# Optimization experiments

Hardware: AMD Instinct MI355X
Metric: run time of the kernel (lower is better)

The kernel has to match this reference:

```python
import jax, jax.numpy as jnp
import numpy as np

BS, M, CLIP_DIM = 64, 1000, 512
D = 512
N_WAYS = 20
N_Z = 8


def setup_inputs() -> dict:
    key = jax.random.key(0)
    ks = jax.random.split(key, 16)
    s = 0.02
    inp = {
        "x_context": jax.random.normal(ks[0], (BS, M, CLIP_DIM), jnp.float32),
        "y_context": jax.random.randint(ks[1], (BS, M), 0, N_WAYS),
        "x_query": jax.random.normal(ks[2], (BS, M, CLIP_DIM), jnp.float32),
        # image_proj
        "Wp": jax.random.normal(ks[3], (CLIP_DIM, D), jnp.float32) * s,
        "bp": jnp.zeros((D,), jnp.float32),
        # aggregator: Linear(d,d) -> GELU -> Linear(d,2d)
        "Wa1": jax.random.normal(ks[4], (D, D), jnp.float32) * s,
        "ba1": jnp.zeros((D,), jnp.float32),
        "Wa2": jax.random.normal(ks[5], (D, 2 * D), jnp.float32) * s,
        "ba2": jnp.zeros((2 * D,), jnp.float32),
        # decoder: Linear(d,d) -> GELU -> Linear(d,d)
        "Wd1": jax.random.normal(ks[6], (D, D), jnp.float32) * s,
        "bd1": jnp.zeros((D,), jnp.float32),
        "Wd2": jax.random.normal(ks[7], (D, D), jnp.float32) * s,
        "bd2": jnp.zeros((D,), jnp.float32),
    }
    return inp


def reference(x_context, y_context, x_query, Wp, bp, Wa1, ba1, Wa2, ba2, Wd1, bd1, Wd2, bd2):
    # project image embeddings: [bs, M, clip_dim] -> [bs, M, d]
    xc = x_context @ Wp + bp
    xq = x_query @ Wp + bp

    # encode_context_per_class: per-class masked sum == one-hot segment-sum
    # (original loops over classes doing (x*mask).sum(dim=1))
    oh = jax.nn.one_hot(y_context, N_WAYS, dtype=xc.dtype)  # [bs, M, N]
    r_C = jnp.einsum('bmn,bmd->bnd', oh, xc)  # [bs, N, d]

    # knowledge is None -> k = zeros; combined = relu(r + 0)
    combined = jax.nn.relu(r_C)
    h = jax.nn.gelu(combined @ Wa1 + ba1, approximate=False)
    stats = h @ Wa2 + ba2  # [bs, N, 2d]
    mu, scale_raw = stats[..., :D], stats[..., D:]
    scale = 0.01 + 0.99 * jax.nn.softplus(scale_raw)

    # eval path: sample n_z from q(z|C) via reparameterization
    eps = jax.random.normal(jax.random.key(42), (N_Z,) + mu.shape, mu.dtype)
    z_samples = mu[None] + scale[None] * eps  # [n_z, bs, N, d]

    # decode: class weight vectors then inner product with queries
    W = jax.nn.gelu(z_samples @ Wd1 + bd1, approximate=False) @ Wd2 + bd2
    logits = jnp.einsum('bqd,sbnd->sbqn', xq, W)  # [n_z, bs, Q*N, N]
    return logits, z_samples, mu, scale
```

## Files before the change

kernel.cpp:

```cpp
#include <hip/hip_runtime.h>
#include <hip/hip_bf16.h>
#include <stdint.h>


typedef __attribute__((ext_vector_type(8))) short short8;
typedef __attribute__((ext_vector_type(4))) float f32x4;

__device__ __forceinline__ float gelu_f(float x) {
    return 0.5f * x * (1.0f + erff(x * 0.70710678118654752440f));
}
__device__ __forceinline__ float softplus_f(float x) {
    return fmaxf(x, 0.0f) + log1pf(expf(-fabsf(x)));
}
__device__ __forceinline__ uint32_t cvt2(float a, float b) {
    __hip_bfloat162 h;
    h.x = __float2bfloat16(a);
    h.y = __float2bfloat16(b);
    uint32_t u; __builtin_memcpy(&u, &h, 4); return u;
}
__device__ __forceinline__ unsigned short f2bfu(float f) {
    __hip_bfloat16 h = __float2bfloat16(f);
    unsigned short u; __builtin_memcpy(&u, &h, 2); return u;
}
__device__ __forceinline__ float bfu2f(unsigned short u) {
    uint32_t v = (uint32_t)u << 16; float f; __builtin_memcpy(&f, &v, 4); return f;
}

__device__ __forceinline__ void threefry2x32(uint32_t k0, uint32_t k1,
                                             uint32_t x0, uint32_t x1,
                                             uint32_t& o0, uint32_t& o1) {
    uint32_t ks[3] = {k0, k1, k0 ^ k1 ^ 0x1BD11BDAu};
    x0 += ks[0]; x1 += ks[1];
    const uint32_t rot[8] = {13,15,26,6,17,29,16,24};
#pragma unroll
    for (int i = 0; i < 5; i++) {
#pragma unroll
        for (int j = 0; j < 4; j++) {
            uint32_t r = rot[(i & 1) * 4 + j];
            x0 += x1;
            x1 = (x1 << r) | (x1 >> (32 - r));
            x1 ^= x0;
        }
        x0 += ks[(i + 1) % 3];
        x1 += ks[(i + 2) % 3] + (uint32_t)(i + 1);
    }
    o0 = x0; o1 = x1;
}

__device__ __forceinline__ float bits_to_normal(uint32_t b) {
    float f = __uint_as_float((b >> 9) | 0x3F800000u) - 1.0f;
    const float lo = __uint_as_float(0xBF7FFFFFu);
    float u = fmaxf(lo, f * 2.0f + lo);
    return 1.41421356237309504880f * erfinvf(u);
}

__global__ __launch_bounds__(256) void prep_k(
    const float* __restrict__ Wp, const float* __restrict__ Wa1,
    const float* __restrict__ Wa2, const float* __restrict__ Wd1,
    const float* __restrict__ Wd2, const float* __restrict__ bp,
    const float* __restrict__ bd2, const int* __restrict__ y,
    unsigned short* __restrict__ WpTb, unsigned short* __restrict__ Wa1Tb,
    unsigned short* __restrict__ Wa2Tb, unsigned short* __restrict__ WdT1b,
    unsigned short* __restrict__ Wpb, unsigned short* __restrict__ Wd2b,
    float* __restrict__ bv, float* __restrict__ w2bp,
    float* __restrict__ c0, float* __restrict__ cnt)
{
    __shared__ float T[64][65];
    __shared__ int lc[32];
    __shared__ float ws4[4];
    const int f = blockIdx.x;
    const int tid = threadIdx.x;

    if (f < 320) {
        const float* src; unsigned short* dst; int C, t, xb, yb;
        if (f < 64)       { src = Wp;  dst = WpTb;  C = 512;  t = f;       xb = t & 7;  yb = t >> 3; }
        else if (f < 128) { src = Wa1; dst = Wa1Tb; C = 512;  t = f - 64;  xb = t & 7;  yb = t >> 3; }
        else if (f < 256) { src = Wa2; dst = Wa2Tb; C = 1024; t = f - 128; xb = t & 15; yb = t >> 4; }
        else              { src = Wd1; dst = WdT1b; C = 512;  t = f - 256; xb = t & 7;  yb = t >> 3; }
        const int r0 = yb * 64, cc0 = xb * 64;
        const int rr = tid >> 4, cc = (tid & 15) * 4;
#pragma unroll
        for (int l = 0; l < 4; l++) {
            int row = rr + l * 16;
            float4 v = *(const float4*)&src[(size_t)(r0 + row) * C + cc0 + cc];
            T[row][cc] = v.x; T[row][cc+1] = v.y; T[row][cc+2] = v.z; T[row][cc+3] = v.w;
        }
        __syncthreads();
#pragma unroll
        for (int l = 0; l < 4; l++) {
            int n = rr + l * 16;
            uint2 u;
            u.x = cvt2(T[cc][n], T[cc+1][n]);
            u.y = cvt2(T[cc+2][n], T[cc+3][n]);
            *(uint2*)&dst[(size_t)(cc0 + n) * 512 + r0 + cc] = u;
        }
    } else if (f < 576) {
        const float* src = (f < 448) ? Wp : Wd2;
        unsigned short* dst = (f < 448) ? Wpb : Wd2b;
        int t = (f < 448) ? f - 320 : f - 448;
        size_t i = ((size_t)t * 256 + tid) * 8;
        float4 a = *(const float4*)&src[i];
        float4 b4 = *(const float4*)&src[i + 4];
        uint4 u;
        u.x = cvt2(a.x, a.y);  u.y = cvt2(a.z, a.w);
        u.z = cvt2(b4.x, b4.y); u.w = cvt2(b4.z, b4.w);
        *(uint4*)&dst[i] = u;
    } else if (f < 832) {
        const float* W = (f < 704) ? Wp : Wd2;
        const float* v = (f < 704) ? bd2 : bp;
        float* o = (f < 704) ? bv : w2bp;
        int t = (f < 704) ? f - 576 : f - 704;
        int wave = tid >> 6, lane = tid & 63;
        int r = t * 4 + wave;
        const float* row = W + (size_t)r * 512 + lane * 8;
        float4 x0 = *(const float4*)row;
        float4 x1 = *(const float4*)(row + 4);
        float4 v0 = *(const float4*)&v[lane * 8];
        float4 v1 = *(const float4*)&v[lane * 8 + 4];
        float s = x0.x*v0.x + x0.y*v0.y + x0.z*v0.z + x0.w*v0.w
                + x1.x*v1.x + x1.y*v1.y + x1.z*v1.z + x1.w*v1.w;
#pragma unroll
        for (int off = 32; off > 0; off >>= 1) s += __shfl_down(s, off, 64);
        if (lane == 0) o[r] = s;
    } else if (f == 832) {
        float s = bp[tid] * bd2[tid] + bp[tid + 256] * bd2[tid + 256];
#pragma unroll
        for (int off = 32; off > 0; off >>= 1) s += __shfl_down(s, off, 64);
        int wave = tid >> 6, lane = tid & 63;
        if (lane == 0) ws4[wave] = s;
        __syncthreads();
        if (tid == 0) c0[0] = ws4[0] + ws4[1] + ws4[2] + ws4[3];
    } else {
        int b = f - 833;
        if (tid < 32) lc[tid] = 0;
        __syncthreads();
        for (int m = tid; m < 1000; m += 256)
            atomicAdd(&lc[y[b * 1000 + m]], 1);
        __syncthreads();
        if (tid < 20) cnt[b * 20 + tid] = (float)lc[tid];
    }
}

__global__ __launch_bounds__(256) void onehot_k(const float* __restrict__ xc,
                                                const int* __restrict__ y,
                                                unsigned short* __restrict__ Abf) {
    __shared__ unsigned short Xs[128 * 64];
    __shared__ int ys[1024];
    const int chb = blockIdx.x * 128;
    const int b = blockIdx.y;
    const int tid = threadIdx.x, lane = tid & 63, w = tid >> 6;
    const int chs = w * 32;

    for (int i = tid; i < 1024; i += 256)
        ys[i] = (i < 1000) ? y[b * 1000 + i] : -1;

    f32x4 acc[2][2] = {};
    for (int step = 0; step < 16; step++) {
        const int k0 = step * 64;
        int m = k0 + lane; if (m > 999) m = 999;
        const float* src = xc + ((size_t)b * 1000 + m) * 512 + chb + chs;
        float x[32];
#pragma unroll
        for (int j8 = 0; j8 < 8; j8++) {
            float4 v = *(const float4*)(src + j8 * 4);
            x[j8*4+0]=v.x; x[j8*4+1]=v.y; x[j8*4+2]=v.z; x[j8*4+3]=v.w;
        }
        __syncthreads();
#pragma unroll
        for (int j = 0; j < 32; j++) {
            int ch = chs + j;
            *(unsigned short*)((char*)Xs + ch * 128 + ((lane * 2) ^ ((ch & 7) << 4)))
                = f2bfu(x[j]);
        }
        __syncthreads();
#pragma unroll
        for (int ks = 0; ks < 2; ks++) {
            int kb = ks * 32 + (lane >> 4) * 8;
            int4 yv0 = *(const int4*)&ys[k0 + kb];
            int4 yv1 = *(const int4*)&ys[k0 + kb + 4];
            int ya[8] = {yv0.x, yv0.y, yv0.z, yv0.w, yv1.x, yv1.y, yv1.z, yv1.w};
            short8 a[2];
#pragma unroll
            for (int mi = 0; mi < 2; mi++) {
                int cls = mi * 16 + (lane & 15);
#pragma unroll
                for (int e = 0; e < 8; e++)
                    a[mi][e] = (short)((ya[e] == cls) ? 0x3F80 : 0);
            }
            short8 bb[2];
#pragma unroll
            for (int ni = 0; ni < 2; ni++) {
                int ch = chs + ni * 16 + (lane & 15);
                bb[ni] = *(const short8*)((const char*)Xs + ch * 128 +
                           ((kb * 2) ^ ((ch & 7) << 4)));
            }
#pragma unroll
            for (int mi = 0; mi < 2; mi++)
#pragma unroll
                for (int ni = 0; ni < 2; ni++)
                    acc[mi][ni] = __builtin_amdgcn_mfma_f32_16x16x32_bf16(a[mi], bb[ni], acc[mi][ni], 0, 0, 0);
        }
    }
#pragma unroll
    for (int mi = 0; mi < 2; mi++) {
#pragma unroll
        for (int ni = 0; ni < 2; ni++) {
            int ch = chb + chs + ni * 16 + (lane & 15);
#pragma unroll
            for (int j = 0; j < 4; j++) {
                int cls = mi * 16 + (lane >> 4) * 4 + j;
                if (cls < 20)
                    Abf[((size_t)b * 20 + cls) * 512 + ch] = f2bfu(acc[mi][ni][j]);
            }
        }
    }
}

template <int EPI>
__global__ __launch_bounds__(256) void gm2_k(const unsigned short* __restrict__ Abf,
                                             const unsigned short* __restrict__ Bbf,
                                             const float* __restrict__ bias,
                                             const float* __restrict__ extra,
                                             unsigned short* __restrict__ C0,
                                             float* __restrict__ F0,
                                             float* __restrict__ F1,
                                             int Nn) {
    __shared__ unsigned short As[64 * 64];
    __shared__ unsigned short Bs[128 * 64];
    const int tid = threadIdx.x;
    const int lane = tid & 63, w = tid >> 6;
    const int row0 = blockIdx.y * 64, col0 = blockIdx.x * 128;
    f32x4 acc[4][2] = {};
    for (int k0 = 0; k0 < 512; k0 += 64) {
        {
            int row = tid >> 2, cs = (tid & 3) * 16;
            int swz = (row & 7) << 4;
            const unsigned short* src = Abf + (size_t)(row0 + row) * 512 + k0 + cs;
#pragma unroll
            for (int j = 0; j < 2; j++) {
                uint4 u = *(const uint4*)(src + j * 8);
                *(uint4*)((char*)As + row * 128 + (((cs + j * 8) * 2) ^ swz)) = u;
            }
        }
        {
            int row = tid >> 1, cs = (tid & 1) * 32;
            int swz = (row & 7) << 4;
            const unsigned short* src = Bbf + (size_t)(col0 + row) * 512 + k0 + cs;
#pragma unroll
            for (int j = 0; j < 4; j++) {
                uint4 u = *(const uint4*)(src + j * 8);
                *(uint4*)((char*)Bs + row * 128 + (((cs + j * 8) * 2) ^ swz)) = u;
            }
        }
        __syncthreads();
#pragma unroll
        for (int ks = 0; ks < 2; ks++) {
            short8 a[4], bb[2];
#pragma unroll
            for (int mi = 0; mi < 4; mi++) {
                int r = mi * 16 + (lane & 15);
                a[mi] = *(const short8*)((const char*)As + r * 128 +
                          (((ks * 32 + (lane >> 4) * 8) * 2) ^ ((r & 7) << 4)));
            }
#pragma unroll
            for (int ni = 0; ni < 2; ni++) {
                int n = w * 32 + ni * 16 + (lane & 15);
                bb[ni] = *(const short8*)((const char*)Bs + n * 128 +
                          (((ks * 32 + (lane >> 4) * 8) * 2) ^ ((n & 7) << 4)));
            }
#pragma unroll
            for (int mi = 0; mi < 4; mi++)
#pragma unroll
                for (int ni = 0; ni < 2; ni++)
                    acc[mi][ni] = __builtin_amdgcn_mfma_f32_16x16x32_bf16(a[mi], bb[ni], acc[mi][ni], 0, 0, 0);
        }
        __syncthreads();
    }
#pragma unroll
    for (int mi = 0; mi < 4; mi++) {
#pragma unroll
        for (int ni = 0; ni < 2; ni++) {
            int c = col0 + w * 32 + ni * 16 + (lane & 15);
            float bvv = bias ? bias[c] : 0.f;
#pragma unroll
            for (int j = 0; j < 4; j++) {
                int r = row0 + mi * 16 + (lane >> 4) * 4 + j;
                float v = acc[mi][ni][j];
                if (EPI == 0) {
                    v += bvv;
                    C0[(size_t)r * Nn + c] = f2bfu(v);
                } else if (EPI == 1) {
                    v += extra[r] * bvv;
                    C0[(size_t)r * Nn + c] = f2bfu(fmaxf(v, 0.f));
                } else if (EPI == 2) {
                    C0[(size_t)r * Nn + c] = f2bfu(gelu_f(v + bvv));
                } else {
                    v += bvv;
                    if (c < 512) F0[(size_t)r * 512 + c] = v;
                    else F1[(size_t)r * 512 + (c - 512)] = 0.01f + 0.99f * softplus_f(v);
                }
            }
        }
    }
}

__global__ __launch_bounds__(256) void z2_k(const float* __restrict__ mu,
                                            const float* __restrict__ sc,
                                            float* __restrict__ z,
                                            unsigned short* __restrict__ zb) {
    const uint32_t NH = 2621440u;
    uint32_t i = blockIdx.x * 256u + threadIdx.x;
    if (i >= NH) return;
    uint32_t t0 = 2u * i;
    uint32_t o0, o1, p0, p1;
    threefry2x32(0u, 42u, 0u, t0, o0, o1);
    threefry2x32(0u, 42u, 0u, t0 + 1u, p0, p1);
    uint32_t r0 = t0 % 655360u;
    float2 mv = *(const float2*)&mu[r0];
    float2 sv = *(const float2*)&sc[r0];
    float z0 = mv.x + sv.x * bits_to_normal(o0 ^ o1);
    float z1 = mv.y + sv.y * bits_to_normal(p0 ^ p1);
    float2 zo; zo.x = z0; zo.y = z1;
    *(float2*)&z[t0] = zo;
    *(uint32_t*)&zb[t0] = cvt2(z0, z1);
}

__global__ __launch_bounds__(256) void beta2_k(const unsigned short* __restrict__ Wgb,
                                               const float* __restrict__ vec,
                                               const float* __restrict__ c0,
                                               float* __restrict__ beta) {
    int wave = threadIdx.x >> 6, lane = threadIdx.x & 63;
    int r = blockIdx.x * 4 + wave;
    short8 wv = *(const short8*)(Wgb + (size_t)r * 512 + lane * 8);
    float s = 0.f;
#pragma unroll
    for (int e = 0; e < 8; e++) s += vec[lane * 8 + e] * bfu2f((unsigned short)wv[e]);
#pragma unroll
    for (int o = 32; o > 0; o >>= 1) s += __shfl_down(s, o, 64);
    if (lane == 0) beta[r] = s + c0[0];
}

__global__ __launch_bounds__(512) void logits_mfma3_k(const float* __restrict__ Xq,
                                                      const unsigned short* __restrict__ Vb,
                                                      const float* __restrict__ beta,
                                                      float* __restrict__ out) {
    __shared__ unsigned short Vs[160 * 64];
    __shared__ float bs[160];
    const int u = blockIdx.x + 8 * blockIdx.y;
    const int xcd = u & 7, idx = u >> 3;
    const int b = (idx & 7) * 8 + xcd;
    const int qh = idx >> 3;
    const int tid = threadIdx.x, lane = tid & 63, w = tid >> 6;
    const int wq = w >> 1, wn = w & 1;

    if (tid < 160) {
        int s = tid / 20, n = tid - s * 20;
        bs[tid] = beta[(size_t)(s * 64 + b) * 20 + n];
    }

    const int klane = (lane >> 4) * 8;
    const float* xp[2];
    int qb[2];
#pragma unroll
    for (int qs = 0; qs < 2; qs++) {
        qb[qs] = qh * 128 + wq * 32 + qs * 16;
        int qr = qb[qs] + (lane & 15);
        if (qr > 999) qr = 999;
        xp[qs] = Xq + ((size_t)b * 1000 + qr) * 512 + klane;
    }
    int vrow[5], vswz[5];
#pragma unroll
    for (int nf = 0; nf < 5; nf++) {
        int rr = wn * 80 + nf * 16 + (lane & 15);
        vrow[nf] = rr * 128;
        vswz[nf] = (rr & 7) << 4;
    }

    f32x4 acc[2][5] = {};
    for (int k0 = 0; k0 < 512; k0 += 64) {
        __syncthreads();
        for (int c = tid; c < 640; c += 512) {
            int row = c >> 2, off = (c & 3) * 32;
            int sdiv = row / 20;
            int row_g = row + sdiv * 1260 + b * 20;
            const unsigned short* src = Vb + (size_t)row_g * 512 + k0 + (c & 3) * 16;
            uint4 u0 = *(const uint4*)src;
            uint4 u1 = *(const uint4*)(src + 8);
            int swz = (row & 7) << 4;
            char* base = (char*)Vs + row * 128;
            *(uint4*)(base + (off ^ swz)) = u0;
            *(uint4*)(base + ((off + 16) ^ swz)) = u1;
        }
        __syncthreads();
#pragma unroll
        for (int ks = 0; ks < 2; ks++) {
            int kb = (ks * 32 + klane) * 2;
            short8 bf[5];
#pragma unroll
            for (int nf = 0; nf < 5; nf++)
                bf[nf] = *(const short8*)((const char*)Vs + vrow[nf] + (kb ^ vswz[nf]));
            short8 af[2];
#pragma unroll
            for (int qs = 0; qs < 2; qs++) {
                const float* p = xp[qs] + k0 + ks * 32;
                float4 v0 = *(const float4*)p;
                float4 v1 = *(const float4*)(p + 4);
                uint4 uu;
                uu.x = cvt2(v0.x, v0.y); uu.y = cvt2(v0.z, v0.w);
                uu.z = cvt2(v1.x, v1.y); uu.w = cvt2(v1.z, v1.w);
                __builtin_memcpy(&af[qs], &uu, 16);
            }
#pragma unroll
            for (int qs = 0; qs < 2; qs++)
#pragma unroll
                for (int nf = 0; nf < 5; nf++)
                    acc[qs][nf] = __builtin_amdgcn_mfma_f32_16x16x32_bf16(af[qs], bf[nf], acc[qs][nf], 0, 0, 0);
        }
    }

#pragma unroll
    for (int nf = 0; nf < 5; nf++) {
        int rl = wn * 80 + nf * 16 + (lane & 15);
        int s = rl / 20, n = rl - s * 20;
        float bb = bs[rl];
        size_t ob = (size_t)(s * 64 + b) * 20000;
#pragma unroll
        for (int qs = 0; qs < 2; qs++) {
#pragma unroll
            for (int j = 0; j < 4; j++) {
                int q = qb[qs] + (lane >> 4) * 4 + j;
                if (q < 1000)
                    out[ob + (size_t)q * 20 + n] = acc[qs][nf][j] + bb;
            }
        }
    }
}

extern "C" void kernel_launch(void* const* d_in, const int* in_sizes, int n_in,
                              void* d_out, int out_size, void* d_ws, size_t ws_size,
                              hipStream_t stream) {
    const float* x_context = (const float*)d_in[0];
    const int*   y_context = (const int*)d_in[1];
    const float* x_query   = (const float*)d_in[2];
    const float* Wp  = (const float*)d_in[3];
    const float* bp  = (const float*)d_in[4];
    const float* Wa1 = (const float*)d_in[5];
    const float* ba1 = (const float*)d_in[6];
    const float* Wa2 = (const float*)d_in[7];
    const float* ba2 = (const float*)d_in[8];
    const float* Wd1 = (const float*)d_in[9];
    const float* bd1 = (const float*)d_in[10];
    const float* Wd2 = (const float*)d_in[11];
    const float* bd2 = (const float*)d_in[12];

    float* out    = (float*)d_out;
    float* logits = out;
    float* z      = out + 10240000;
    float* mu     = out + 15482880;
    float* sc     = out + 16138240;

    float* ws   = (float*)d_ws;
    float* cnt  = ws;
    float* beta = cnt + 1280;
    float* bv   = beta + 10240;
    float* w2bp = bv + 512;
    float* c0   = w2bp + 512;
    unsigned short* WpTb  = (unsigned short*)(c0 + 63);
    unsigned short* Wa1Tb = WpTb + 262144;
    unsigned short* Wa2Tb = Wa1Tb + 262144;
    unsigned short* WdT1b = Wa2Tb + 524288;
    unsigned short* Wpb   = WdT1b + 262144;
    unsigned short* Wd2b  = Wpb + 262144;
    unsigned short* Gtb   = Wd2b + 262144;
    unsigned short* Abf   = Gtb + 262144;
    unsigned short* combb = Abf + 655360;
    unsigned short* hb    = combb + 655360;
    unsigned short* zb    = hb + 655360;
    unsigned short* Vbf   = zb + 5242880;
    float* big = (float*)(Vbf + 5242880);
    unsigned short* Wgb = (unsigned short*)big;

    prep_k<<<dim3(897), 256, 0, stream>>>(Wp, Wa1, Wa2, Wd1, Wd2, bp, bd2, y_context,
                                          WpTb, Wa1Tb, Wa2Tb, WdT1b, Wpb, Wd2b,
                                          bv, w2bp, c0, cnt);
    gm2_k<0><<<dim3(4, 8), 256, 0, stream>>>(Wpb, Wd2b, nullptr, nullptr, Gtb, nullptr, nullptr, 512);
    onehot_k<<<dim3(4, 64), 256, 0, stream>>>(x_context, y_context, Abf);
    gm2_k<1><<<dim3(4, 20), 256, 0, stream>>>(Abf, WpTb, bp, cnt, combb, nullptr, nullptr, 512);
    gm2_k<2><<<dim3(4, 20), 256, 0, stream>>>(combb, Wa1Tb, ba1, nullptr, hb, nullptr, nullptr, 512);
    gm2_k<3><<<dim3(8, 20), 256, 0, stream>>>(hb, Wa2Tb, ba2, nullptr, nullptr, mu, sc, 1024);
    z2_k<<<dim3(10240), 256, 0, stream>>>(mu, sc, z, zb);
    gm2_k<2><<<dim3(4, 160), 256, 0, stream>>>(zb, WdT1b, bd1, nullptr, Wgb, nullptr, nullptr, 512);
    gm2_k<0><<<dim3(4, 160), 256, 0, stream>>>(Wgb, Gtb, bv, nullptr, Vbf, nullptr, nullptr, 512);
    beta2_k<<<dim3(2560), 256, 0, stream>>>(Wgb, w2bp, c0, beta);
    logits_mfma3_k<<<dim3(8, 64), 512, 0, stream>>>(x_query, Vbf, beta, logits);
}
```

Before: 232.0 us.

## Split one-hot segment-sum over M chunks and fuse weight conversion into Gt GEMM

The one-hot class-sum kernel now splits the 1000 context rows into four chunks, launching 1024 blocks instead of 256 to raise occupancy. Each chunk writes fp32 partials, and a new reduction kernel sums them and converts to bf16. Separately, the Wp·Wd2 product GEMM now reads fp32 weights directly and converts them to bf16 while loading tiles, removing the separate conversion pass in prep_k. The cost is an extra kernel launch and a partial-sum buffer round-trip through global memory.

```diff
diff --git a/kernel.cpp b/kernel.cpp
--- a/kernel.cpp
+++ b/kernel.cpp
@@ -61,7 +61,6 @@
     const float* __restrict__ bd2, const int* __restrict__ y,
     unsigned short* __restrict__ WpTb, unsigned short* __restrict__ Wa1Tb,
     unsigned short* __restrict__ Wa2Tb, unsigned short* __restrict__ WdT1b,
-    unsigned short* __restrict__ Wpb, unsigned short* __restrict__ Wd2b,
     float* __restrict__ bv, float* __restrict__ w2bp,
     float* __restrict__ c0, float* __restrict__ cnt)
 {
@@ -95,21 +94,10 @@
             *(uint2*)&dst[(size_t)(cc0 + n) * 512 + r0 + cc] = u;
         }
     } else if (f < 576) {
-        const float* src = (f < 448) ? Wp : Wd2;
-        unsigned short* dst = (f < 448) ? Wpb : Wd2b;
+        const float* W = (f < 448) ? Wp : Wd2;
+        const float* v = (f < 448) ? bd2 : bp;
+        float* o = (f < 448) ? bv : w2bp;
         int t = (f < 448) ? f - 320 : f - 448;
-        size_t i = ((size_t)t * 256 + tid) * 8;
-        float4 a = *(const float4*)&src[i];
-        float4 b4 = *(const float4*)&src[i + 4];
-        uint4 u;
-        u.x = cvt2(a.x, a.y);  u.y = cvt2(a.z, a.w);
-        u.z = cvt2(b4.x, b4.y); u.w = cvt2(b4.z, b4.w);
-        *(uint4*)&dst[i] = u;
-    } else if (f < 832) {
-        const float* W = (f < 704) ? Wp : Wd2;
-        const float* v = (f < 704) ? bd2 : bp;
-        float* o = (f < 704) ? bv : w2bp;
-        int t = (f < 704) ? f - 576 : f - 704;
         int wave = tid >> 6, lane = tid & 63;
         int r = t * 4 + wave;
         const float* row = W + (size_t)r * 512 + lane * 8;
@@ -122,7 +110,7 @@
 #pragma unroll
         for (int off = 32; off > 0; off >>= 1) s += __shfl_down(s, off, 64);
         if (lane == 0) o[r] = s;
-    } else if (f == 832) {
+    } else if (f == 576) {
         float s = bp[tid] * bd2[tid] + bp[tid + 256] * bd2[tid + 256];
 #pragma unroll
         for (int off = 32; off > 0; off >>= 1) s += __shfl_down(s, off, 64);
@@ -131,7 +119,7 @@
         __syncthreads();
         if (tid == 0) c0[0] = ws4[0] + ws4[1] + ws4[2] + ws4[3];
     } else {
-        int b = f - 833;
+        int b = f - 577;
         if (tid < 32) lc[tid] = 0;
         __syncthreads();
         for (int m = tid; m < 1000; m += 256)
@@ -141,23 +129,102 @@
     }
 }
 
-__global__ __launch_bounds__(256) void onehot_k(const float* __restrict__ xc,
-                                                const int* __restrict__ y,
-                                                unsigned short* __restrict__ Abf) {
+__global__ __launch_bounds__(256) void gmG_k(const float* __restrict__ Ap,
+                                             const float* __restrict__ Bp,
+                                             unsigned short* __restrict__ C) {
+    __shared__ unsigned short As[64 * 64];
+    __shared__ unsigned short Bs[128 * 64];
+    const int tid = threadIdx.x;
+    const int lane = tid & 63, w = tid >> 6;
+    const int row0 = blockIdx.y * 64, col0 = blockIdx.x * 128;
+    f32x4 acc[4][2] = {};
+    for (int k0 = 0; k0 < 512; k0 += 64) {
+        {
+            int row = tid >> 2, cs = (tid & 3) * 16;
+            int swz = (row & 7) << 4;
+            const float* src = Ap + (size_t)(row0 + row) * 512 + k0 + cs;
+#pragma unroll
+            for (int j = 0; j < 2; j++) {
+                float4 v0 = *(const float4*)(src + j * 8);
+                float4 v1 = *(const float4*)(src + j * 8 + 4);
+                uint4 u;
+                u.x = cvt2(v0.x, v0.y); u.y = cvt2(v0.z, v0.w);
+                u.z = cvt2(v1.x, v1.y); u.w = cvt2(v1.z, v1.w);
+                *(uint4*)((char*)As + row * 128 + (((cs + j * 8) * 2) ^ swz)) = u;
+            }
+        }
+        {
+            int row = tid >> 1, cs = (tid & 1) * 32;
+            int swz = (row & 7) << 4;
+            const float* src = Bp + (size_t)(col0 + row) * 512 + k0 + cs;
+#pragma unroll
+            for (int j = 0; j < 4; j++) {
+                float4 v0 = *(const float4*)(src + j * 8);
+                float4 v1 = *(const float4*)(src + j * 8 + 4);
+                uint4 u;
+                u.x = cvt2(v0.x, v0.y); u.y = cvt2(v0.z, v0.w);
+                u.z = cvt2(v1.x, v1.y); u.w = cvt2(v1.z, v1.w);
+                *(uint4*)((char*)Bs + row * 128 + (((cs + j * 8) * 2) ^ swz)) = u;
+            }
+        }
+        __syncthreads();
+#pragma unroll
+        for (int ks = 0; ks < 2; ks++) {
+            short8 a[4], bb[2];
+#pragma unroll
+            for (int mi = 0; mi < 4; mi++) {
+                int r = mi * 16 + (lane & 15);
+                a[mi] = *(const short8*)((const char*)As + r * 128 +
+                          (((ks * 32 + (lane >> 4) * 8) * 2) ^ ((r & 7) << 4)));
+            }
+#pragma unroll
+            for (int ni = 0; ni < 2; ni++) {
+                int n = w * 32 + ni * 16 + (lane & 15);
+                bb[ni] = *(const short8*)((const char*)Bs + n * 128 +
+                          (((ks * 32 + (lane >> 4) * 8) * 2) ^ ((n & 7) << 4)));
+            }
+#pragma unroll
+            for (int mi = 0; mi < 4; mi++)
+#pragma unroll
+                for (int ni = 0; ni < 2; ni++)
+                    acc[mi][ni] = __builtin_amdgcn_mfma_f32_16x16x32_bf16(a[mi], bb[ni], acc[mi][ni], 0, 0, 0);
+        }
+        __syncthreads();
+    }
+#pragma unroll
+    for (int mi = 0; mi < 4; mi++)
+#pragma unroll
+        for (int ni = 0; ni < 2; ni++) {
+            int c = col0 + w * 32 + ni * 16 + (lane & 15);
+#pragma unroll
+            for (int j = 0; j < 4; j++) {
+                int r = row0 + mi * 16 + (lane >> 4) * 4 + j;
+                C[(size_t)r * 512 + c] = f2bfu(acc[mi][ni][j]);
+            }
+        }
+}
+
+__global__ __launch_bounds__(256) void onehot4_k(const float* __restrict__ xc,
+                                                 const int* __restrict__ y,
+                                                 float* __restrict__ Apart) {
     __shared__ unsigned short Xs[128 * 64];
-    __shared__ int ys[1024];
+    __shared__ int ys[256];
     const int chb = blockIdx.x * 128;
-    const int b = blockIdx.y;
+    const int mc = blockIdx.y;
+    const int b = blockIdx.z;
+    const int m00 = mc * 256;
     const int tid = threadIdx.x, lane = tid & 63, w = tid >> 6;
     const int chs = w * 32;
 
-    for (int i = tid; i < 1024; i += 256)
-        ys[i] = (i < 1000) ? y[b * 1000 + i] : -1;
+    {
+        int mg = m00 + tid;
+        ys[tid] = (mg < 1000) ? y[b * 1000 + mg] : -1;
+    }
 
     f32x4 acc[2][2] = {};
-    for (int step = 0; step < 16; step++) {
+    for (int step = 0; step < 4; step++) {
         const int k0 = step * 64;
-        int m = k0 + lane; if (m > 999) m = 999;
+        int m = m00 + k0 + lane; if (m > 999) m = 999;
         const float* src = xc + ((size_t)b * 1000 + m) * 512 + chb + chs;
         float x[32];
 #pragma unroll
@@ -201,6 +268,7 @@
                     acc[mi][ni] = __builtin_amdgcn_mfma_f32_16x16x32_bf16(a[mi], bb[ni], acc[mi][ni], 0, 0, 0);
         }
     }
+    float* dst = Apart + (size_t)mc * 655360;
 #pragma unroll
     for (int mi = 0; mi < 2; mi++) {
 #pragma unroll
@@ -210,9 +278,26 @@
             for (int j = 0; j < 4; j++) {
                 int cls = mi * 16 + (lane >> 4) * 4 + j;
                 if (cls < 20)
-                    Abf[((size_t)b * 20 + cls) * 512 + ch] = f2bfu(acc[mi][ni][j]);
-            }
-        }
+                    dst[((size_t)b * 20 + cls) * 512 + ch] = acc[mi][ni][j];
+            }
+        }
+    }
+}
+
+__global__ __launch_bounds__(256) void reduceA_k(const float* __restrict__ Apart,
+                                                 unsigned short* __restrict__ Abf) {
+    int i = blockIdx.x * 256 + threadIdx.x;
+    if (i < 163840) {
+        const float4* Ap4 = (const float4*)Apart;
+        float4 s = Ap4[i];
+#pragma unroll
+        for (int p = 1; p < 4; p++) {
+            float4 v = Ap4[(size_t)p * 163840 + i];
+            s.x += v.x; s.y += v.y; s.z += v.z; s.w += v.w;
+        }
+        uint2 o;
+        o.x = cvt2(s.x, s.y); o.y = cvt2(s.z, s.w);
+        *(uint2*)&Abf[(size_t)i * 4] = o;
     }
 }
 
@@ -469,9 +554,7 @@
     unsigned short* Wa1Tb = WpTb + 262144;
     unsigned short* Wa2Tb = Wa1Tb + 262144;
     unsigned short* WdT1b = Wa2Tb + 524288;
-    unsigned short* Wpb   = WdT1b + 262144;
-    unsigned short* Wd2b  = Wpb + 262144;
-    unsigned short* Gtb   = Wd2b + 262144;
+    unsigned short* Gtb   = WdT1b + 262144;
     unsigned short* Abf   = Gtb + 262144;
     unsigned short* combb = Abf + 655360;
     unsigned short* hb    = combb + 655360;
@@ -480,11 +563,12 @@
     float* big = (float*)(Vbf + 5242880);
     unsigned short* Wgb = (unsigned short*)big;
 
-    prep_k<<<dim3(897), 256, 0, stream>>>(Wp, Wa1, Wa2, Wd1, Wd2, bp, bd2, y_context,
-                                          WpTb, Wa1Tb, Wa2Tb, WdT1b, Wpb, Wd2b,
+    prep_k<<<dim3(641), 256, 0, stream>>>(Wp, Wa1, Wa2, Wd1, Wd2, bp, bd2, y_context,
+                                          WpTb, Wa1Tb, Wa2Tb, WdT1b,
                                           bv, w2bp, c0, cnt);
-    gm2_k<0><<<dim3(4, 8), 256, 0, stream>>>(Wpb, Wd2b, nullptr, nullptr, Gtb, nullptr, nullptr, 512);
-    onehot_k<<<dim3(4, 64), 256, 0, stream>>>(x_context, y_context, Abf);
+    gmG_k<<<dim3(4, 8), 256, 0, stream>>>(Wp, Wd2, Gtb);
+    onehot4_k<<<dim3(4, 4, 64), 256, 0, stream>>>(x_context, y_context, big);
+    reduceA_k<<<dim3(640), 256, 0, stream>>>(big, Abf);
     gm2_k<1><<<dim3(4, 20), 256, 0, stream>>>(Abf, WpTb, bp, cnt, combb, nullptr, nullptr, 512);
     gm2_k<2><<<dim3(4, 20), 256, 0, stream>>>(combb, Wa1Tb, ba1, nullptr, hb, nullptr, nullptr, 512);
     gm2_k<3><<<dim3(8, 20), 256, 0, stream>>>(hb, Wa2Tb, ba2, nullptr, nullptr, mu, sc, 1024);
```

Measured after the change: 236.0 us. No clear change (+1.7%).
